# Performance work log

Hardware: AMD Instinct MI355X
Metric: run time of the kernel (lower is better)

## Reference

```python
import jax, jax.numpy as jnp
import numpy as np
from jax import lax

WS = 8      # window size (square)
SS = 4      # shift size
HEADS = 8
K = 9       # snake-conv kernel size
CENTER = K // 2
EXT = 1.0   # extend_scope


def _shift_attn_mask(H, W):
    # static numpy construction of Swin shift mask -> [num_windows, L, L]
    m = np.zeros((H, W), dtype=np.float32)
    cnt = 0
    for hs in [(0, -WS), (-WS, -SS), (-SS, None)]:
        for ws_ in [(0, -WS), (-WS, -SS), (-SS, None)]:
            m[hs[0]:hs[1], ws_[0]:ws_[1]] = cnt
            cnt += 1
    m = m.reshape(H // WS, WS, W // WS, WS).transpose(0, 2, 1, 3).reshape(-1, WS * WS)
    d = m[:, None, :] - m[:, :, None]
    return jnp.asarray(np.where(d != 0, -100.0, 0.0).astype(np.float32))


def shifted_window_attention(x, qkv_w, qkv_b, proj_w, proj_b, rel_bias):
    B, H, W, C = x.shape
    d = C // HEADS
    x = jnp.roll(x, shift=(-SS, -SS), axis=(1, 2))
    nH, nW = H // WS, W // WS
    nwin, L = nH * nW, WS * WS
    # window partition -> [B*nwin, L, C]
    xw = x.reshape(B, nH, WS, nW, WS, C).transpose(0, 1, 3, 2, 4, 5).reshape(B * nwin, L, C)
    qkv = (xw @ qkv_w.T + qkv_b).reshape(B * nwin, L, 3, HEADS, d).transpose(2, 0, 3, 1, 4)
    q, k, v = qkv[0] * (d ** -0.5), qkv[1], qkv[2]
    attn = jnp.einsum('nhld,nhmd->nhlm', q, k) + rel_bias[None]
    amask = _shift_attn_mask(H, W)  # [nwin, L, L]
    attn = attn.reshape(B, nwin, HEADS, L, L) + amask[None, :, None]
    attn = jax.nn.softmax(attn.reshape(B * nwin, HEADS, L, L), axis=-1)
    out = jnp.einsum('nhlm,nhmd->nhld', attn, v).transpose(0, 2, 1, 3).reshape(B * nwin, L, C)
    out = out @ proj_w.T + proj_b
    out = out.reshape(B, nH, nW, WS, WS, C).transpose(0, 1, 3, 2, 4, 5).reshape(B, H, W, C)
    return jnp.roll(out, shift=(SS, SS), axis=(1, 2))


def snake_coordinate_map(offset):
    # offset [B, 2K, Wd, Hd], morph=0: cumulative y offsets from the kernel center
    B, _, Wd, Hd = offset.shape
    y_off = offset[:, :K]
    # y_new[center]=0; y_new[center+i]=sum_{j=1..i} y_off[center+j]; mirror below
    up = jnp.cumsum(y_off[:, CENTER + 1:], axis=1)
    down = jnp.cumsum(y_off[:, :CENTER][:, ::-1], axis=1)[:, ::-1]
    y_cum = jnp.concatenate([down, jnp.zeros((B, 1, Wd, Hd), offset.dtype), up], axis=1)
    y_center = jnp.arange(Wd, dtype=offset.dtype)[None, None, :, None]
    y_new = y_center + EXT * y_cum                              # [B,K,Wd,Hd]
    x_spread = jnp.linspace(-CENTER, CENTER, K, dtype=offset.dtype)[None, :, None, None]
    x_center = jnp.arange(Hd, dtype=offset.dtype)[None, None, None, :]
    x_new = jnp.broadcast_to(x_center + x_spread, (B, K, Wd, Hd))
    # rearrange 'b k w h -> b (w k) h'
    y_map = y_new.transpose(0, 2, 1, 3).reshape(B, Wd * K, Hd)
    x_map = x_new.transpose(0, 2, 1, 3).reshape(B, Wd * K, Hd)
    return y_map, x_map


def bilinear_sample(feat, ymap, xmap):
    Hin, Win = feat.shape[-2], feat.shape[-1]
    y = jnp.clip(ymap, 0.0, Hin - 1.0)
    x = jnp.clip(xmap, 0.0, Win - 1.0)
    y0f, x0f = jnp.floor(y), jnp.floor(x)
    wy, wx = y - y0f, x - x0f
    y0 = y0f.astype(jnp.int32); x0 = x0f.astype(jnp.int32)
    y1 = jnp.minimum(y0 + 1, Hin - 1); x1 = jnp.minimum(x0 + 1, Win - 1)
    g = jax.vmap(lambda f, yy, xx: f[:, yy, xx])  # -> [B,C,Ho,Wo]
    v00 = g(feat, y0, x0); v01 = g(feat, y0, x1)
    v10 = g(feat, y1, x0); v11 = g(feat, y1, x1)
    wy = wy[:, None]; wx = wx[:, None]
    return v00 * (1 - wy) * (1 - wx) + v01 * (1 - wy) * wx + v10 * wy * (1 - wx) + v11 * wy * wx


def _forward(x, qkv_weight, qkv_bias, proj_weight, proj_bias, rel_bias, offset, dsc_weight, dsc_bias):
    y = shifted_window_attention(x, qkv_weight, qkv_bias, proj_weight, proj_bias, rel_bias)
    feat = y.transpose(0, 3, 1, 2)                      # NCHW
    ymap, xmap = snake_coordinate_map(offset)
    samp = bilinear_sample(feat, ymap, xmap)            # [B,C,H*K,W]
    out = lax.conv_general_dilated(samp, dsc_weight, window_strides=(K, 1), padding='VALID',
                                   dimension_numbers=('NCHW', 'OIHW', 'NCHW'))
    return jax.nn.relu(out + dsc_bias[None, :, None, None])


def setup_inputs() -> dict:
    key = jax.random.key(0)
    ks = jax.random.split(key, 9)
    B, H, W, C = 8, 64, 64, 256
    return {
        'x': jax.random.normal(ks[0], (B, H, W, C), jnp.float32),
        'qkv_weight': jax.random.normal(ks[1], (3 * C, C), jnp.float32) * 0.05,
        'qkv_bias': jax.random.normal(ks[2], (3 * C,), jnp.float32) * 0.05,
        'proj_weight': jax.random.normal(ks[3], (C, C), jnp.float32) * 0.05,
        'proj_bias': jax.random.normal(ks[4], (C,), jnp.float32) * 0.05,
        'rel_bias': jax.random.normal(ks[5], (HEADS, WS * WS, WS * WS), jnp.float32) * 0.05,
        'offset': jax.random.normal(ks[6], (B, 2 * K, H, W), jnp.float32),
        'dsc_weight': jax.random.normal(ks[7], (C, C, K, 1), jnp.float32) * 0.02,
        'dsc_bias': jax.random.normal(ks[8], (C,), jnp.float32) * 0.02,
    }


def reference(x, qkv_weight, qkv_bias, proj_weight, proj_bias, rel_bias, offset, dsc_weight, dsc_bias):
    return _forward(x, qkv_weight, qkv_bias, proj_weight, proj_bias, rel_bias, offset, dsc_weight, dsc_bias)
```

## Files before the change

kernel.cpp:

```cpp
#include <hip/hip_runtime.h>
#include <math.h>


#define NFLOAT_BUF 8388608

typedef float f32x4 __attribute__((ext_vector_type(4)));
typedef __bf16 bf16x8 __attribute__((ext_vector_type(8)));
typedef _Float16 f16x8 __attribute__((ext_vector_type(8)));

__device__ inline unsigned pack2_bf16(float a, float b) {
    union { float f; unsigned u; } ua, ub;
    ua.f = a; ub.f = b;
    unsigned ra = (ua.u + 0x7FFFu + ((ua.u >> 16) & 1u)) >> 16;
    unsigned rb = (ub.u + 0x7FFFu + ((ub.u >> 16) & 1u)) & 0xFFFF0000u;
    return (ra & 0xFFFFu) | rb;
}

__global__ __launch_bounds__(256) void prep_kernel(
    const float* __restrict__ x, unsigned short* __restrict__ xb,
    const float* __restrict__ qkv_w, unsigned short* __restrict__ wb,
    const float* __restrict__ proj_w, _Float16* __restrict__ pwh,
    const float* __restrict__ dsc_w, _Float16* __restrict__ wT,
    const float* __restrict__ offset, float* __restrict__ ymap) {
    int bid = blockIdx.x, tid = threadIdx.x;
    if (bid < 4096) {
        int t = bid * 256 + tid;
        const float4* s = (const float4*)(x + (size_t)t * 8);
        float4 a = s[0], b = s[1];
        uint4 o;
        o.x = pack2_bf16(a.x, a.y); o.y = pack2_bf16(a.z, a.w);
        o.z = pack2_bf16(b.x, b.y); o.w = pack2_bf16(b.z, b.w);
        *(uint4*)(xb + (size_t)t * 8) = o;
    } else if (bid < 4192) {
        int t = (bid - 4096) * 256 + tid;
        if (t < 24576) {
            const float4* s = (const float4*)(qkv_w + (size_t)t * 8);
            float4 a = s[0], b = s[1];
            uint4 o;
            o.x = pack2_bf16(a.x, a.y); o.y = pack2_bf16(a.z, a.w);
            o.z = pack2_bf16(b.x, b.y); o.w = pack2_bf16(b.z, b.w);
            *(uint4*)(wb + (size_t)t * 8) = o;
        }
    } else if (bid < 4224) {
        int t = (bid - 4192) * 256 + tid;
        if (t < 8192) {
            const float4* s = (const float4*)(proj_w + (size_t)t * 8);
            float4 a = s[0], b = s[1];
            union { _Float16 h[8]; uint4 u; } o;
            o.h[0] = (_Float16)a.x; o.h[1] = (_Float16)a.y;
            o.h[2] = (_Float16)a.z; o.h[3] = (_Float16)a.w;
            o.h[4] = (_Float16)b.x; o.h[5] = (_Float16)b.y;
            o.h[6] = (_Float16)b.z; o.h[7] = (_Float16)b.w;
            *(uint4*)(pwh + (size_t)t * 8) = o.u;
        }
    } else if (bid < 6528) {
        int t = (bid - 4224) * 256 + tid;
        int o = t / 2304;
        int kk = t - o * 2304;
        int k = kk >> 8, i = kk & 255;
        wT[t] = (_Float16)dsc_w[(o * 256 + i) * 9 + k];
    } else {
        int t = (bid - 6528) * 256 + tid;
        int hd = t & 63;
        int wd = (t >> 6) & 63;
        int b  = t >> 12;
        const float* op = offset + ((size_t)(b * 18) * 64 + wd) * 64 + hd;
        float yo[9];
        #pragma unroll
        for (int k = 0; k < 9; ++k) yo[k] = op[(size_t)k * 4096];
        float cum[9];
        cum[4] = 0.0f;
        float s = 0.0f;
        for (int j = 3; j >= 0; --j) { s += yo[j]; cum[j] = s; }
        s = 0.0f;
        for (int j = 5; j < 9; ++j) { s += yo[j]; cum[j] = s; }
        float wdf = (float)wd;
        float* yp = ymap + ((size_t)(b * 576 + wd * 9)) * 64 + hd;
        #pragma unroll
        for (int k = 0; k < 9; ++k) yp[(size_t)k * 64] = wdf + cum[k];
    }
}

__global__ __launch_bounds__(512, 2) void qkv_mfma2_kernel(
    const unsigned short* __restrict__ xb, const unsigned short* __restrict__ wb,
    const float* __restrict__ qkv_b,
    _Float16* __restrict__ qh, _Float16* __restrict__ kh, _Float16* __restrict__ vt) {

    __shared__ __align__(16) char SH[98816];
    char* Ab[2] = { SH, SH + 16384 };
    char* Bb[2] = { SH + 32768, SH + 65536 };
    unsigned* rowoff = (unsigned*)(SH + 98304);

    int nb = blockIdx.x;
    int m0 = blockIdx.y * 128;
    int gw0 = m0 >> 6;
    int tid = threadIdx.x;
    int lane = tid & 63, w = tid >> 6;
    int qc = lane & 15, g = lane >> 4;
    int ph = w >> 2, nq = w & 3;

    if (tid < 128) {
        int l = tid;
        int gw = gw0 + (l >> 6);
        int b = gw >> 6, win = gw & 63;
        int l2 = l & 63;
        int rh = ((win >> 3) << 3) + (l2 >> 3);
        int rw = ((win & 7) << 3) + (l2 & 7);
        int sh_ = (rh + 4) & 63, sw_ = (rw + 4) & 63;
        rowoff[l] = (unsigned)(((b * 64 + sh_) * 64 + sw_) * 512);
    }

    f32x4 acc[4][4];
    #pragma unroll
    for (int m = 0; m < 4; ++m)
        #pragma unroll
        for (int n = 0; n < 4; ++n) {
            f32x4 z = {0.0f, 0.0f, 0.0f, 0.0f};
            acc[m][n] = z;
        }

    const char* xc = (const char*)xb;
    const char* wc = (const char*)wb;
    int rAa = qc * 128;
    int u0 = ((g    ) ^ (qc & 7)) << 4;
    int u1 = ((4 + g) ^ (qc & 7)) << 4;

    __syncthreads();

    #pragma unroll
    for (int r = 0; r < 2; ++r) {
        int pos = r * 512 + tid;
        int row = pos >> 3, u = pos & 7;
        const char* src = xc + rowoff[row] + ((u ^ (row & 7)) << 4);
        __builtin_amdgcn_global_load_lds(
            (const __attribute__((address_space(1))) unsigned int*)src,
            (__attribute__((address_space(3))) unsigned int*)(Ab[0] + pos * 16),
            16, 0, 0);
    }
    #pragma unroll
    for (int r = 0; r < 4; ++r) {
        int pos = r * 512 + tid;
        int n = pos >> 3, u = pos & 7;
        const char* src = wc + (size_t)(nb * 256 + n) * 512 + ((u ^ (n & 7)) << 4);
        __builtin_amdgcn_global_load_lds(
            (const __attribute__((address_space(1))) unsigned int*)src,
            (__attribute__((address_space(3))) unsigned int*)(Bb[0] + pos * 16),
            16, 0, 0);
    }
    __syncthreads();

    for (int c = 0; c < 4; ++c) {
        int cur = c & 1, nxt = cur ^ 1;

        if (c < 3) {
            int cn = c + 1;
            #pragma unroll
            for (int r = 0; r < 2; ++r) {
                int pos = r * 512 + tid;
                int row = pos >> 3, u = pos & 7;
                const char* src = xc + rowoff[row] + cn * 128 + ((u ^ (row & 7)) << 4);
                __builtin_amdgcn_global_load_lds(
                    (const __attribute__((address_space(1))) unsigned int*)src,
                    (__attribute__((address_space(3))) unsigned int*)(Ab[nxt] + pos * 16),
                    16, 0, 0);
            }
            #pragma unroll
            for (int r = 0; r < 4; ++r) {
                int pos = r * 512 + tid;
                int n = pos >> 3, u = pos & 7;
                const char* src = wc + (size_t)(nb * 256 + n) * 512 + cn * 128 + ((u ^ (n & 7)) << 4);
                __builtin_amdgcn_global_load_lds(
                    (const __attribute__((address_space(1))) unsigned int*)src,
                    (__attribute__((address_space(3))) unsigned int*)(Bb[nxt] + pos * 16),
                    16, 0, 0);
            }
        }

        bf16x8 av[4][2], bv[4][2];
        #pragma unroll
        for (int m = 0; m < 4; ++m) {
            char* abase = Ab[cur] + ph * 8192 + m * 2048 + rAa;
            av[m][0] = *(const bf16x8*)(abase + u0);
            av[m][1] = *(const bf16x8*)(abase + u1);
        }
        #pragma unroll
        for (int n = 0; n < 4; ++n) {
            char* bbase = Bb[cur] + nq * 8192 + n * 2048 + rAa;
            bv[n][0] = *(const bf16x8*)(bbase + u0);
            bv[n][1] = *(const bf16x8*)(bbase + u1);
        }
        #pragma unroll
        for (int m = 0; m < 4; ++m)
            #pragma unroll
            for (int n = 0; n < 4; ++n) {
                acc[m][n] = __builtin_amdgcn_mfma_f32_16x16x32_bf16(av[m][0], bv[n][0], acc[m][n], 0, 0, 0);
                acc[m][n] = __builtin_amdgcn_mfma_f32_16x16x32_bf16(av[m][1], bv[n][1], acc[m][n], 0, 0, 0);
            }
        __syncthreads();
    }

    if (nb == 2) {
        #pragma unroll
        for (int n = 0; n < 4; ++n) {
            int o = nq * 64 + n * 16 + qc;
            float bias = qkv_b[512 + o];
            int hh = o >> 5, dd = o & 31;
            _Float16* base = vt + ((size_t)((gw0 + ph) * 8 + hh) * 32 + dd) * 64;
            #pragma unroll
            for (int m = 0; m < 4; ++m) {
                int l0 = m * 16 + g * 4;
                union { _Float16 x[4]; uint2 u; } pk;
                #pragma unroll
                for (int j = 0; j < 4; ++j) pk.x[j] = (_Float16)(acc[m][n][j] + bias);
                *(uint2*)(base + l0) = pk.u;
            }
        }
    } else {
        float scale = (nb == 0) ? 0.17677669529663689f : 1.0f;
        char* eL = SH + 32768;
        #pragma unroll
        for (int n = 0; n < 4; ++n) {
            int f = nq * 64 + n * 16 + qc;
            float bias = qkv_b[nb * 256 + f];
            int slot = f >> 3, fin = (f & 7) * 2;
            #pragma unroll
            for (int m = 0; m < 4; ++m)
                #pragma unroll
                for (int j = 0; j < 4; ++j) {
                    int l = ph * 64 + m * 16 + g * 4 + j;
                    *(_Float16*)(eL + l * 512 + ((slot ^ (l & 7)) << 4) + fin) =
                        (_Float16)((acc[m][n][j] + bias) * scale);
                }
        }
        __syncthreads();
        _Float16* dstb = (nb == 0) ? qh : kh;
        #pragma unroll
        for (int r = 0; r < 8; ++r) {
            int s = r * 512 + tid;
            int h = s >> 9, l = (s >> 2) & 127, p = s & 3;
            uint4 vdat = *(const uint4*)(eL + l * 512 + (((h * 4 + p) ^ (l & 7)) << 4));
            int gw = gw0 + (l >> 6);
            *(uint4*)(dstb + ((size_t)(gw * 8 + h) * 64 + (l & 63)) * 32 + p * 8) = vdat;
        }
    }
}

__global__ __launch_bounds__(512, 4) void attn_proj_kernel(
    const _Float16* __restrict__ qh, const _Float16* __restrict__ kh,
    const _Float16* __restrict__ vt, const float* __restrict__ rel_bias,
    const _Float16* __restrict__ pwh, const float* __restrict__ proj_b,
    _Float16* __restrict__ feath) {

    __shared__ __align__(16) char SH[65536];
    int n = blockIdx.x;
    int win = n & 63;
    int wy = win >> 3, wx = win & 7;
    int tid = threadIdx.x, lane = tid & 63, h = tid >> 6;
    int qc = lane & 15, g = lane >> 4;
    char* P = SH + h * 8192;

    const _Float16* qp = qh + (size_t)(n * 8 + h) * 2048;
    const _Float16* kp = kh + (size_t)(n * 8 + h) * 2048;
    const _Float16* vp = vt + (size_t)(n * 8 + h) * 2048;
    const float* rb = rel_bias + (size_t)h * 4096;

    int rk[16];
    #pragma unroll
    for (int mt = 0; mt < 4; ++mt)
        #pragma unroll
        for (int j = 0; j < 4; ++j) {
            int key = mt * 16 + g * 4 + j;
            int rh = wy * 8 + (key >> 3), rw = wx * 8 + (key & 7);
            rk[mt * 4 + j] = (rh < 56 ? 0 : (rh < 60 ? 1 : 2)) * 3
                           + (rw < 56 ? 0 : (rw < 60 ? 1 : 2));
        }

    f16x8 kf[4];
    #pragma unroll
    for (int mt = 0; mt < 4; ++mt)
        kf[mt] = *(const f16x8*)(kp + (mt * 16 + qc) * 32 + g * 8);

    #pragma unroll
    for (int nt = 0; nt < 4; ++nt) {
        int q = nt * 16 + qc;
        int rqh = wy * 8 + (q >> 3), rqw = wx * 8 + (q & 7);
        int rq = (rqh < 56 ? 0 : (rqh < 60 ? 1 : 2)) * 3
               + (rqw < 56 ? 0 : (rqw < 60 ? 1 : 2));
        f16x8 qf = *(const f16x8*)(qp + q * 32 + g * 8);

        f32x4 s[4];
        #pragma unroll
        for (int mt = 0; mt < 4; ++mt) {
            f32x4 z = {0.0f, 0.0f, 0.0f, 0.0f};
            s[mt] = __builtin_amdgcn_mfma_f32_16x16x32_f16(kf[mt], qf, z, 0, 0, 0);
        }

        float vals[16];
        #pragma unroll
        for (int mt = 0; mt < 4; ++mt) {
            float4 bv4 = *(const float4*)(rb + q * 64 + mt * 16 + g * 4);
            vals[mt * 4 + 0] = s[mt][0] + bv4.x + (rk[mt * 4 + 0] != rq ? -100.0f : 0.0f);
            vals[mt * 4 + 1] = s[mt][1] + bv4.y + (rk[mt * 4 + 1] != rq ? -100.0f : 0.0f);
            vals[mt * 4 + 2] = s[mt][2] + bv4.z + (rk[mt * 4 + 2] != rq ? -100.0f : 0.0f);
            vals[mt * 4 + 3] = s[mt][3] + bv4.w + (rk[mt * 4 + 3] != rq ? -100.0f : 0.0f);
        }

        float mx = vals[0];
        #pragma unroll
        for (int i = 1; i < 16; ++i) mx = fmaxf(mx, vals[i]);
        mx = fmaxf(mx, __shfl_xor(mx, 16));
        mx = fmaxf(mx, __shfl_xor(mx, 32));

        float sum = 0.0f;
        #pragma unroll
        for (int i = 0; i < 16; ++i) { vals[i] = __expf(vals[i] - mx); sum += vals[i]; }
        sum += __shfl_xor(sum, 16);
        sum += __shfl_xor(sum, 32);
        float inv = 1.0f / sum;

        #pragma unroll
        for (int mt = 0; mt < 4; ++mt) {
            union { _Float16 x[4]; uint2 u; } pk4;
            #pragma unroll
            for (int j = 0; j < 4; ++j) pk4.x[j] = (_Float16)(vals[mt * 4 + j] * inv);
            int off = (mt * 32 + g * 8) ^ ((q & 7) << 4);
            *(uint2*)(P + q * 128 + off) = pk4.u;
        }
    }

    f16x8 pa[4][2];
    #pragma unroll
    for (int im = 0; im < 4; ++im)
        #pragma unroll
        for (int ks = 0; ks < 2; ++ks) {
            int row = im * 16 + qc;
            int off = (ks * 64 + g * 16) ^ ((row & 7) << 4);
            pa[im][ks] = *(const f16x8*)(P + row * 128 + off);
        }
    f16x8 bvv[2][2];
    #pragma unroll
    for (int in = 0; in < 2; ++in)
        #pragma unroll
        for (int ks = 0; ks < 2; ++ks)
            bvv[in][ks] = *(const f16x8*)(vp + (in * 16 + qc) * 64 + ks * 32 + g * 8);

    f32x4 acc[4][2];
    #pragma unroll
    for (int im = 0; im < 4; ++im)
        #pragma unroll
        for (int in = 0; in < 2; ++in) {
            f32x4 z = {0.0f, 0.0f, 0.0f, 0.0f};
            acc[im][in] = z;
        }
    #pragma unroll
    for (int im = 0; im < 4; ++im)
        #pragma unroll
        for (int in = 0; in < 2; ++in) {
            acc[im][in] = __builtin_amdgcn_mfma_f32_16x16x32_f16(pa[im][0], bvv[in][0], acc[im][in], 0, 0, 0);
            acc[im][in] = __builtin_amdgcn_mfma_f32_16x16x32_f16(pa[im][1], bvv[in][1], acc[im][in], 0, 0, 0);
        }

    __syncthreads();

    char* aob = SH;
    char* Bsb = SH + 32768;
    #pragma unroll
    for (int im = 0; im < 4; ++im)
        #pragma unroll
        for (int in = 0; in < 2; ++in)
            #pragma unroll
            for (int j = 0; j < 4; ++j) {
                int row = im * 16 + g * 4 + j;
                int f = h * 32 + in * 16 + qc;
                *(_Float16*)(aob + row * 512 + ((((f >> 3) ^ (row & 7)) << 4) + (f & 7) * 2)) =
                    (_Float16)acc[im][in][j];
            }
    __syncthreads();

    int w04 = h & 3, wm = h >> 2;
    const char* wcp = (const char*)pwh;
    int bidx = n >> 6;

    f32x4 pacc[2][4];
    #pragma unroll
    for (int m = 0; m < 2; ++m)
        #pragma unroll
        for (int nn = 0; nn < 4; ++nn) {
            f32x4 z = {0.0f, 0.0f, 0.0f, 0.0f};
            pacc[m][nn] = z;
        }

    for (int c = 0; c < 4; ++c) {
        #pragma unroll
        for (int r = 0; r < 4; ++r) {
            int pos = r * 512 + tid;
            int nr = pos >> 3, uu = pos & 7;
            const char* src = wcp + (size_t)nr * 512 + c * 128 + ((uu ^ (nr & 7)) << 4);
            __builtin_amdgcn_global_load_lds(
                (const __attribute__((address_space(1))) unsigned int*)src,
                (__attribute__((address_space(3))) unsigned int*)(Bsb + pos * 16),
                16, 0, 0);
        }
        __syncthreads();

        f16x8 av2[2][2], bv2[4][2];
        #pragma unroll
        for (int m = 0; m < 2; ++m) {
            int row = wm * 32 + m * 16 + qc;
            #pragma unroll
            for (int ks = 0; ks < 2; ++ks) {
                int u = c * 8 + ks * 4 + g;
                av2[m][ks] = *(const f16x8*)(aob + row * 512 + ((u ^ (row & 7)) << 4));
            }
        }
        #pragma unroll
        for (int nn = 0; nn < 4; ++nn) {
            int oc = w04 * 64 + nn * 16 + qc;
            #pragma unroll
            for (int ks = 0; ks < 2; ++ks)
                bv2[nn][ks] = *(const f16x8*)(Bsb + oc * 128 + (((ks * 4 + g) ^ (oc & 7)) << 4));
        }
        #pragma unroll
        for (int m = 0; m < 2; ++m)
            #pragma unroll
            for (int nn = 0; nn < 4; ++nn) {
                pacc[m][nn] = __builtin_amdgcn_mfma_f32_16x16x32_f16(av2[m][0], bv2[nn][0], pacc[m][nn], 0, 0, 0);
                pacc[m][nn] = __builtin_amdgcn_mfma_f32_16x16x32_f16(av2[m][1], bv2[nn][1], pacc[m][nn], 0, 0, 0);
            }
        __syncthreads();
    }

    #pragma unroll
    for (int nn = 0; nn < 4; ++nn) {
        int f = w04 * 64 + nn * 16 + qc;
        float bias = proj_b[f];
        #pragma unroll
        for (int m = 0; m < 2; ++m) {
            #pragma unroll
            for (int j = 0; j < 4; ++j) {
                int px = wm * 32 + m * 16 + g * 4 + j;
                int rh = ((win >> 3) << 3) + (px >> 3);
                int rw = ((win & 7) << 3) + (px & 7);
                int p = (rh + 4) & 63;
                int qq = (rw + 4) & 63;
                feath[((size_t)(bidx * 64 + p) * 64 + qq) * 256 + f] =
                    (_Float16)(pacc[m][nn][j] + bias);
            }
        }
    }
}

__global__ __launch_bounds__(512) void sample_conv_mfma4_kernel(
    const _Float16* __restrict__ feath, const float* __restrict__ ymap,
    const _Float16* __restrict__ wT2h, const float* __restrict__ dsc_b,
    float* __restrict__ out) {

    __shared__ __align__(16) char Ab[2][16384];
    __shared__ __align__(16) char Bb[2][32768];
    __shared__ unsigned row0[2][9][64];
    __shared__ unsigned row1[2][9][64];
    __shared__ float    wyv[2][9][64];

    int blk = blockIdx.x;
    int b = blk & 7, wd0 = (blk >> 3) * 2;
    int tid = threadIdx.x;
    int lane = tid & 63, w = tid >> 6;
    int qc = lane & 15, g = lane >> 4;
    int ph = w >> 2, nq = w & 3;

    for (int idx = tid; idx < 1152; idx += 512) {
        int wdl = idx / 576;
        int r = idx - wdl * 576;
        int k = r >> 6, hd = r & 63;
        int wd = wd0 + wdl;
        float y = ymap[((size_t)(b * 576 + wd * 9 + k)) * 64 + hd];
        y = fminf(fmaxf(y, 0.0f), 63.0f);
        float y0f = floorf(y);
        int y0 = (int)y0f;
        int y1 = min(y0 + 1, 63);
        int xc = min(max(hd + k - 4, 0), 63);
        row0[wdl][k][hd] = (unsigned)(((b * 64 + y0) * 64 + xc) * 512);
        row1[wdl][k][hd] = (unsigned)(((b * 64 + y1) * 64 + xc) * 512);
        wyv[wdl][k][hd] = y - y0f;
    }

    f32x4 acc[4][4];
    #pragma unroll
    for (int m = 0; m < 4; ++m)
        #pragma unroll
        for (int n = 0; n < 4; ++n) {
            f32x4 z = {0.0f, 0.0f, 0.0f, 0.0f};
            acc[m][n] = z;
        }

    const char* featc = (const char*)feath;
    const char* wc    = (const char*)wT2h;

    int pxA[2], sAv[2];
    #pragma unroll
    for (int r = 0; r < 2; ++r) {
        int pos = r * 512 + tid;
        pxA[r] = pos >> 3;
        sAv[r] = pos & 7;
    }

    int rAa = qc * 128;
    int u0 = ((g    ) ^ (qc & 7)) << 4;
    int u1 = ((4 + g) ^ (qc & 7)) << 4;

    __syncthreads();

    #pragma unroll
    for (int r = 0; r < 4; ++r) {
        int pos = r * 512 + tid;
        int n = pos >> 3, uu = pos & 7;
        const char* src = wc + n * 4608 + 0 * 128 + ((uu ^ (n & 7)) << 4);
        __builtin_amdgcn_global_load_lds(
            (const __attribute__((address_space(1))) unsigned int*)src,
            (__attribute__((address_space(3))) unsigned int*)(Bb[0] + pos * 16),
            16, 0, 0);
    }
    #pragma unroll
    for (int r = 0; r < 2; ++r) {
        int px = pxA[r], sA = sAv[r];
        int wdl = px >> 6, hd = px & 63;
        unsigned b0 = row0[wdl][0][hd] + sA * 16;
        unsigned b1 = row1[wdl][0][hd] + sA * 16;
        float wy = wyv[wdl][0][hd];
        f16x8 v0 = *(const f16x8*)(featc + b0);
        f16x8 v1 = *(const f16x8*)(featc + b1);
        _Float16 wyh = (_Float16)wy;
        _Float16 omh = (_Float16)(1.0f - wy);
        f16x8 res = v0 * omh + v1 * wyh;
        *(f16x8*)(Ab[0] + px * 128 + ((sA ^ (px & 7)) << 4)) = res;
    }
    __syncthreads();

    for (int c = 0; c < 36; ++c) {
        int cur = c & 1, nxt = cur ^ 1;

        f16x8 s0[2], s1[2];
        float swy[2];
        if (c < 35) {
            int cn = c + 1;
            int ks = cn >> 2, cib = (cn & 3) * 128;
            #pragma unroll
            for (int r = 0; r < 4; ++r) {
                int pos = r * 512 + tid;
                int n = pos >> 3, uu = pos & 7;
                const char* src = wc + n * 4608 + cn * 128 + ((uu ^ (n & 7)) << 4);
                __builtin_amdgcn_global_load_lds(
                    (const __attribute__((address_space(1))) unsigned int*)src,
                    (__attribute__((address_space(3))) unsigned int*)(Bb[nxt] + pos * 16),
                    16, 0, 0);
            }
            #pragma unroll
            for (int r = 0; r < 2; ++r) {
                int px = pxA[r], sA = sAv[r];
                int wdl = px >> 6, hd = px & 63;
                unsigned b0 = row0[wdl][ks][hd] + cib + sA * 16;
                unsigned b1 = row1[wdl][ks][hd] + cib + sA * 16;
                swy[r] = wyv[wdl][ks][hd];
                s0[r] = *(const f16x8*)(featc + b0);
                s1[r] = *(const f16x8*)(featc + b1);
            }
        }

        f16x8 av[4][2], bv[4][2];
        #pragma unroll
        for (int m = 0; m < 4; ++m) {
            char* abase = Ab[cur] + ph * 8192 + m * 2048 + rAa;
            av[m][0] = *(const f16x8*)(abase + u0);
            av[m][1] = *(const f16x8*)(abase + u1);
        }
        #pragma unroll
        for (int n = 0; n < 4; ++n) {
            char* bbase = Bb[cur] + nq * 8192 + n * 2048 + rAa;
            bv[n][0] = *(const f16x8*)(bbase + u0);
            bv[n][1] = *(const f16x8*)(bbase + u1);
        }
        #pragma unroll
        for (int m = 0; m < 4; ++m)
            #pragma unroll
            for (int n = 0; n < 4; ++n) {
                acc[m][n] = __builtin_amdgcn_mfma_f32_16x16x32_f16(av[m][0], bv[n][0], acc[m][n], 0, 0, 0);
                acc[m][n] = __builtin_amdgcn_mfma_f32_16x16x32_f16(av[m][1], bv[n][1], acc[m][n], 0, 0, 0);
            }

        if (c < 35) {
            #pragma unroll
            for (int r = 0; r < 2; ++r) {
                int px = pxA[r], sA = sAv[r];
                _Float16 wyh = (_Float16)swy[r];
                _Float16 omh = (_Float16)(1.0f - swy[r]);
                f16x8 res = s0[r] * omh + s1[r] * wyh;
                *(f16x8*)(Ab[nxt] + px * 128 + ((sA ^ (px & 7)) << 4)) = res;
            }
        }
        __syncthreads();
    }

    #pragma unroll
    for (int n = 0; n < 4; ++n) {
        int o = nq * 64 + n * 16 + qc;
        float bvs = dsc_b[o];
        float* orow = out + ((size_t)(b * 256 + o) * 64 + (wd0 + ph)) * 64;
        #pragma unroll
        for (int m = 0; m < 4; ++m) {
            int px = m * 16 + g * 4;
            float4 res;
            res.x = fmaxf(acc[m][n][0] + bvs, 0.0f);
            res.y = fmaxf(acc[m][n][1] + bvs, 0.0f);
            res.z = fmaxf(acc[m][n][2] + bvs, 0.0f);
            res.w = fmaxf(acc[m][n][3] + bvs, 0.0f);
            *(float4*)(orow + px) = res;
        }
    }
}

extern "C" void kernel_launch(void* const* d_in, const int* in_sizes, int n_in,
                              void* d_out, int out_size, void* d_ws, size_t ws_size,
                              hipStream_t stream) {
    (void)in_sizes; (void)n_in; (void)out_size; (void)ws_size;
    const float* x        = (const float*)d_in[0];
    const float* qkv_w    = (const float*)d_in[1];
    const float* qkv_b    = (const float*)d_in[2];
    const float* proj_w   = (const float*)d_in[3];
    const float* proj_b   = (const float*)d_in[4];
    const float* rel_bias = (const float*)d_in[5];
    const float* offset   = (const float*)d_in[6];
    const float* dsc_w    = (const float*)d_in[7];
    const float* dsc_b    = (const float*)d_in[8];
    float* out = (float*)d_out;

    unsigned short* wsu = (unsigned short*)d_ws;
    _Float16* qh = (_Float16*)wsu;
    _Float16* kh = (_Float16*)(wsu + NFLOAT_BUF);
    _Float16* vt = (_Float16*)(wsu + 2 * (size_t)NFLOAT_BUF);
    _Float16* feath = (_Float16*)(wsu + 3 * (size_t)NFLOAT_BUF);
    unsigned short* xb      = wsu + 4 * (size_t)NFLOAT_BUF;
    unsigned short* wb      = wsu + 5 * (size_t)NFLOAT_BUF;
    _Float16* pwh           = (_Float16*)(wb + 196608);
    _Float16* wT2h          = (_Float16*)((unsigned short*)pwh + 65536);
    float* ymap = (float*)((unsigned short*)wT2h + 589824);

    prep_kernel<<<6656, 256, 0, stream>>>(x, xb, qkv_w, wb, proj_w, pwh,
                                          dsc_w, wT2h, offset, ymap);
    qkv_mfma2_kernel<<<dim3(3, 256), 512, 0, stream>>>(xb, wb, qkv_b, qh, kh, vt);
    attn_proj_kernel<<<512, 512, 0, stream>>>(qh, kh, vt, rel_bias, pwh, proj_b, feath);
    sample_conv_mfma4_kernel<<<256, 512, 0, stream>>>(feath, ymap, wT2h, dsc_b, out);
}
```

Baseline: 208.2 us.

## Double-buffer projection weight tiles and hoist Q/K/V loads in attention kernel

The attention+projection kernel now prefetches the first proj-weight chunk into LDS at kernel start and double-buffers later chunks, so each chunk's global-to-LDS copy overlaps the MFMA work on the previous one. Q, K and V fragments are all loaded up front instead of inside the loops. The prep kernel's dsc weight transpose now reads the source coalesced and scatters the writes. In exchange, LDS per block doubles to 128KB and the minimum-occupancy hint is dropped, which likely leaves one block per CU instead of two and reduces latency hiding across blocks.

```diff
diff --git a/kernel.cpp b/kernel.cpp
--- a/kernel.cpp
+++ b/kernel.cpp
@@ -57,8 +57,9 @@
         int t = (bid - 4224) * 256 + tid;
         int o = t / 2304;
         int kk = t - o * 2304;
-        int k = kk >> 8, i = kk & 255;
-        wT[t] = (_Float16)dsc_w[(o * 256 + i) * 9 + k];
+        int i = kk / 9;
+        int k = kk - i * 9;
+        wT[o * 2304 + k * 256 + i] = (_Float16)dsc_w[t];
     } else {
         int t = (bid - 6528) * 256 + tid;
         int hd = t & 63;
@@ -245,24 +246,50 @@
     }
 }
 
-__global__ __launch_bounds__(512, 4) void attn_proj_kernel(
+__global__ __launch_bounds__(512) void attn_proj_kernel(
     const _Float16* __restrict__ qh, const _Float16* __restrict__ kh,
     const _Float16* __restrict__ vt, const float* __restrict__ rel_bias,
     const _Float16* __restrict__ pwh, const float* __restrict__ proj_b,
     _Float16* __restrict__ feath) {
 
-    __shared__ __align__(16) char SH[65536];
+    __shared__ __align__(16) char SH[131072];
     int n = blockIdx.x;
     int win = n & 63;
     int wy = win >> 3, wx = win & 7;
     int tid = threadIdx.x, lane = tid & 63, h = tid >> 6;
     int qc = lane & 15, g = lane >> 4;
     char* P = SH + h * 8192;
+    char* Bdb[2] = { SH + 65536, SH + 98304 };
 
     const _Float16* qp = qh + (size_t)(n * 8 + h) * 2048;
     const _Float16* kp = kh + (size_t)(n * 8 + h) * 2048;
     const _Float16* vp = vt + (size_t)(n * 8 + h) * 2048;
     const float* rb = rel_bias + (size_t)h * 4096;
+    const char* wcp = (const char*)pwh;
+
+    f16x8 kf[4], qf4[4], bvv[2][2];
+    #pragma unroll
+    for (int mt = 0; mt < 4; ++mt)
+        kf[mt] = *(const f16x8*)(kp + (mt * 16 + qc) * 32 + g * 8);
+    #pragma unroll
+    for (int nt = 0; nt < 4; ++nt)
+        qf4[nt] = *(const f16x8*)(qp + (nt * 16 + qc) * 32 + g * 8);
+    #pragma unroll
+    for (int in = 0; in < 2; ++in)
+        #pragma unroll
+        for (int ks = 0; ks < 2; ++ks)
+            bvv[in][ks] = *(const f16x8*)(vp + (in * 16 + qc) * 64 + ks * 32 + g * 8);
+
+    #pragma unroll
+    for (int r = 0; r < 4; ++r) {
+        int pos = r * 512 + tid;
+        int nr = pos >> 3, uu = pos & 7;
+        const char* src = wcp + (size_t)nr * 512 + ((uu ^ (nr & 7)) << 4);
+        __builtin_amdgcn_global_load_lds(
+            (const __attribute__((address_space(1))) unsigned int*)src,
+            (__attribute__((address_space(3))) unsigned int*)(Bdb[0] + pos * 16),
+            16, 0, 0);
+    }
 
     int rk[16];
     #pragma unroll
@@ -275,24 +302,18 @@
                            + (rw < 56 ? 0 : (rw < 60 ? 1 : 2));
         }
 
-    f16x8 kf[4];
-    #pragma unroll
-    for (int mt = 0; mt < 4; ++mt)
-        kf[mt] = *(const f16x8*)(kp + (mt * 16 + qc) * 32 + g * 8);
-
     #pragma unroll
     for (int nt = 0; nt < 4; ++nt) {
         int q = nt * 16 + qc;
         int rqh = wy * 8 + (q >> 3), rqw = wx * 8 + (q & 7);
         int rq = (rqh < 56 ? 0 : (rqh < 60 ? 1 : 2)) * 3
                + (rqw < 56 ? 0 : (rqw < 60 ? 1 : 2));
-        f16x8 qf = *(const f16x8*)(qp + q * 32 + g * 8);
 
         f32x4 s[4];
         #pragma unroll
         for (int mt = 0; mt < 4; ++mt) {
             f32x4 z = {0.0f, 0.0f, 0.0f, 0.0f};
-            s[mt] = __builtin_amdgcn_mfma_f32_16x16x32_f16(kf[mt], qf, z, 0, 0, 0);
+            s[mt] = __builtin_amdgcn_mfma_f32_16x16x32_f16(kf[mt], qf4[nt], z, 0, 0, 0);
         }
 
         float vals[16];
@@ -337,12 +358,6 @@
             int off = (ks * 64 + g * 16) ^ ((row & 7) << 4);
             pa[im][ks] = *(const f16x8*)(P + row * 128 + off);
         }
-    f16x8 bvv[2][2];
-    #pragma unroll
-    for (int in = 0; in < 2; ++in)
-        #pragma unroll
-        for (int ks = 0; ks < 2; ++ks)
-            bvv[in][ks] = *(const f16x8*)(vp + (in * 16 + qc) * 64 + ks * 32 + g * 8);
 
     f32x4 acc[4][2];
     #pragma unroll
@@ -363,7 +378,6 @@
     __syncthreads();
 
     char* aob = SH;
-    char* Bsb = SH + 32768;
     #pragma unroll
     for (int im = 0; im < 4; ++im)
         #pragma unroll
@@ -378,7 +392,6 @@
     __syncthreads();
 
     int w04 = h & 3, wm = h >> 2;
-    const char* wcp = (const char*)pwh;
     int bidx = n >> 6;
 
     f32x4 pacc[2][4];
@@ -391,17 +404,20 @@
         }
 
     for (int c = 0; c < 4; ++c) {
-        #pragma unroll
-        for (int r = 0; r < 4; ++r) {
-            int pos = r * 512 + tid;
-            int nr = pos >> 3, uu = pos & 7;
-            const char* src = wcp + (size_t)nr * 512 + c * 128 + ((uu ^ (nr & 7)) << 4);
-            __builtin_amdgcn_global_load_lds(
-                (const __attribute__((address_space(1))) unsigned int*)src,
-                (__attribute__((address_space(3))) unsigned int*)(Bsb + pos * 16),
-                16, 0, 0);
-        }
-        __syncthreads();
+        int cur = c & 1;
+        if (c < 3) {
+            int cn = c + 1;
+            #pragma unroll
+            for (int r = 0; r < 4; ++r) {
+                int pos = r * 512 + tid;
+                int nr = pos >> 3, uu = pos & 7;
+                const char* src = wcp + (size_t)nr * 512 + cn * 128 + ((uu ^ (nr & 7)) << 4);
+                __builtin_amdgcn_global_load_lds(
+                    (const __attribute__((address_space(1))) unsigned int*)src,
+                    (__attribute__((address_space(3))) unsigned int*)(Bdb[cur ^ 1] + pos * 16),
+                    16, 0, 0);
+            }
+        }
 
         f16x8 av2[2][2], bv2[4][2];
         #pragma unroll
@@ -418,7 +434,7 @@
             int oc = w04 * 64 + nn * 16 + qc;
             #pragma unroll
             for (int ks = 0; ks < 2; ++ks)
-                bv2[nn][ks] = *(const f16x8*)(Bsb + oc * 128 + (((ks * 4 + g) ^ (oc & 7)) << 4));
+                bv2[nn][ks] = *(const f16x8*)(Bdb[cur] + oc * 128 + (((ks * 4 + g) ^ (oc & 7)) << 4));
         }
         #pragma unroll
         for (int m = 0; m < 2; ++m)
```

Measured after the change: 212.0 us. No clear change (+1.8%).
